# Kernel tuning notes

Hardware: AMD Instinct MI355X
Metric: run time of the kernel (lower is better)

The kernel has to match this reference:

```python
import jax, jax.numpy as jnp
import numpy as np

FP8_MAX = 448.0  # float8_e4m3fn max representable value


def _fp8_quant(v):
    """Snap values to the fp8 e4m3 grid (saturating), return fp32."""
    v = jnp.clip(v, -FP8_MAX, FP8_MAX)
    return v.astype(jnp.float8_e4m3fn).astype(jnp.float32)


def setup_inputs() -> dict:
    key = jax.random.key(0)
    k1, k2, k3 = jax.random.split(key, 3)
    N_TOK, D_IN, D_OUT = 8192, 4096, 4096
    x = jax.random.normal(k1, (N_TOK, D_IN), dtype=jnp.float32)
    # weight is stored already quantized to fp8 in the real module; snap to grid
    w = jax.random.normal(k2, (D_OUT, D_IN), dtype=jnp.float32)
    weight_scale = jnp.array([2.0 / FP8_MAX], dtype=jnp.float32)  # per-tensor
    weight = _fp8_quant(w / weight_scale)  # fp8-grid values, kept in fp32
    bias = jax.random.normal(k3, (D_OUT,), dtype=jnp.float32)
    input_scale = jnp.array([4.0 / FP8_MAX], dtype=jnp.float32)  # per-tensor act scale
    return {"x": x, "weight": weight, "weight_scale": weight_scale,
            "bias": bias, "input_scale": input_scale}


def reference(x, weight, weight_scale, bias, input_scale):
    # quantize_activation_per_tensor_fp8: x/scale -> clamp -> fp8 e4m3
    qinput = _fp8_quant(x / input_scale)  # [N, D_in], fp8-grid values
    acc = jnp.einsum('nk,ok->no', qinput, weight)  # fp32 accumulate
    out = acc * (input_scale * weight_scale) + bias
    return out.astype(x.dtype)
```

## Files before the change

kernel.cpp:

```cpp
#include <hip/hip_runtime.h>
#include <stdint.h>

#define FP8_MAX 448.0f

typedef float floatx4 __attribute__((ext_vector_type(4)));
typedef long  longx2  __attribute__((ext_vector_type(2)));

__device__ __forceinline__ void async_copy16(const void* g, void* s) {
    __builtin_amdgcn_global_load_lds(
        (const __attribute__((address_space(1))) void*)g,
        (__attribute__((address_space(3))) void*)s,
        16, 0, 0);
}

__global__ void __launch_bounds__(256) quant_fp8_kernel(
    const float* __restrict__ src, const float* __restrict__ scale,
    uint8_t* __restrict__ dst, long n16)
{
    long g = (long)blockIdx.x * 256 + threadIdx.x;
    if (g >= n16) return;
    long i = g * 16;
    float inv = 1.0f;
    if (scale) inv = 1.0f / scale[0];
    const float4* p = (const float4*)(src + i);
    int out[4];
#pragma unroll
    for (int j = 0; j < 4; ++j) {
        float4 v = p[j];
        float a = v.x * inv, b = v.y * inv, c = v.z * inv, d = v.w * inv;
        a = fminf(fmaxf(a, -FP8_MAX), FP8_MAX);
        b = fminf(fmaxf(b, -FP8_MAX), FP8_MAX);
        c = fminf(fmaxf(c, -FP8_MAX), FP8_MAX);
        d = fminf(fmaxf(d, -FP8_MAX), FP8_MAX);
        int pk = 0;
        pk = __builtin_amdgcn_cvt_pk_fp8_f32(a, b, pk, false);
        pk = __builtin_amdgcn_cvt_pk_fp8_f32(c, d, pk, true);
        out[j] = pk;
    }
    *(int4*)(dst + i) = make_int4(out[0], out[1], out[2], out[3]);
}

__global__ void __launch_bounds__(256, 2) gemm_fp8_kernel(
    const uint8_t* __restrict__ A, const uint8_t* __restrict__ B,
    const float* __restrict__ bias,
    const float* __restrict__ in_scale, const float* __restrict__ w_scale,
    float* __restrict__ C, int M, int N, int K)
{
    __shared__ __align__(16) uint8_t As[128 * 64];
    __shared__ __align__(16) uint8_t Bs[128 * 64];

    const int tid  = threadIdx.x;
    const int lane = tid & 63;
    const int wid  = tid >> 6;
    const int wm   = wid >> 1;
    const int wn   = wid & 1;
    const int m0   = blockIdx.y * 128;
    const int n0   = blockIdx.x * 128;

    const int mlane = lane & 15;
    const int quad  = lane >> 4;

    const int c0 = tid, c1 = tid + 256;
    const int rA0 = c0 >> 2, cA0 = (c0 & 3) * 16;
    const int rA1 = c1 >> 2, cA1 = (c1 & 3) * 16;

    const uint8_t* Ab = A + (size_t)m0 * K;
    const uint8_t* Bb = B + (size_t)n0 * K;

    floatx4 acc[4][4];
#pragma unroll
    for (int i = 0; i < 4; ++i)
#pragma unroll
        for (int j = 0; j < 4; ++j) acc[i][j] = (floatx4){0.f, 0.f, 0.f, 0.f};

    const int aoff = (wm * 64 + mlane) * 64 + quad * 16;
    const int boff = (wn * 64 + mlane) * 64 + quad * 16;

    for (int kt = 0; kt < K; kt += 64) {
        async_copy16(Ab + (size_t)rA0 * K + kt + cA0, As + c0 * 16);
        async_copy16(Ab + (size_t)rA1 * K + kt + cA1, As + c1 * 16);
        async_copy16(Bb + (size_t)rA0 * K + kt + cA0, Bs + c0 * 16);
        async_copy16(Bb + (size_t)rA1 * K + kt + cA1, Bs + c1 * 16);
        __syncthreads();

        longx2 av[4], bv[4];
#pragma unroll
        for (int mi = 0; mi < 4; ++mi)
            av[mi] = *(const longx2*)(As + aoff + mi * 16 * 64);
#pragma unroll
        for (int ni = 0; ni < 4; ++ni)
            bv[ni] = *(const longx2*)(Bs + boff + ni * 16 * 64);

#pragma unroll
        for (int mi = 0; mi < 4; ++mi)
#pragma unroll
            for (int ni = 0; ni < 4; ++ni)
                acc[mi][ni] = __builtin_amdgcn_mfma_f32_16x16x32_fp8_fp8(
                    av[mi].x, bv[ni].x, acc[mi][ni], 0, 0, 0);
#pragma unroll
        for (int mi = 0; mi < 4; ++mi)
#pragma unroll
            for (int ni = 0; ni < 4; ++ni)
                acc[mi][ni] = __builtin_amdgcn_mfma_f32_16x16x32_fp8_fp8(
                    av[mi].y, bv[ni].y, acc[mi][ni], 0, 0, 0);

        __syncthreads();
    }

    const float osc = in_scale[0] * w_scale[0];

#pragma unroll
    for (int mi = 0; mi < 4; ++mi) {
#pragma unroll
        for (int ni = 0; ni < 4; ++ni) {
            const int gn = n0 + wn * 64 + ni * 16 + mlane;
            const float bvv = bias[gn];
#pragma unroll
            for (int r = 0; r < 4; ++r) {
                const int gm = m0 + wm * 64 + mi * 16 + quad * 4 + r;
                C[(size_t)gm * N + gn] = acc[mi][ni][r] * osc + bvv;
            }
        }
    }
}

extern "C" void kernel_launch(void* const* d_in, const int* in_sizes, int n_in,
                              void* d_out, int out_size, void* d_ws, size_t ws_size,
                              hipStream_t stream) {
    const float* x        = (const float*)d_in[0];
    const float* weight   = (const float*)d_in[1];
    const float* w_scale  = (const float*)d_in[2];
    const float* bias     = (const float*)d_in[3];
    const float* in_scale = (const float*)d_in[4];
    float* out = (float*)d_out;

    const int N = in_sizes[3];
    const int K = in_sizes[1] / N;
    const int M = in_sizes[0] / K;

    uint8_t* qx = (uint8_t*)d_ws;
    uint8_t* qw = (uint8_t*)d_ws + (size_t)M * K;

    const long nx16 = (long)M * K / 16;
    const long nw16 = (long)N * K / 16;
    quant_fp8_kernel<<<(nx16 + 255) / 256, 256, 0, stream>>>(x, in_scale, qx, nx16);
    quant_fp8_kernel<<<(nw16 + 255) / 256, 256, 0, stream>>>(weight, nullptr, qw, nw16);

    dim3 grid(N / 128, M / 128);
    gemm_fp8_kernel<<<grid, 256, 0, stream>>>(qx, qw, bias, in_scale, w_scale,
                                              out, M, N, K);
}
```

Before: 434.3 us.

## Reorder LDS tile layout for conflict-free MFMA reads; grid-stride quant kernel

The GEMM's shared-memory tiles are reorganised so each 16-row by 64-byte MFMA sub-tile sits in a contiguous 1 KB block. Every lane then reads 16 consecutive bytes at lane*16 instead of striding by 64 bytes per row, which is meant to remove LDS bank conflicts on the fragment loads. The global-to-LDS copy mapping is changed to match, which makes each group of 16 threads fetch from 16 different rows. The quantization kernel becomes a grid-stride loop with one float4 per thread and a capped grid, trading wider 16-byte stores for narrower 4-byte stores.

```diff
diff --git a/kernel.cpp b/kernel.cpp
--- a/kernel.cpp
+++ b/kernel.cpp
@@ -15,29 +15,22 @@
 
 __global__ void __launch_bounds__(256) quant_fp8_kernel(
     const float* __restrict__ src, const float* __restrict__ scale,
-    uint8_t* __restrict__ dst, long n16)
+    uint8_t* __restrict__ dst, long n4)
 {
-    long g = (long)blockIdx.x * 256 + threadIdx.x;
-    if (g >= n16) return;
-    long i = g * 16;
     float inv = 1.0f;
     if (scale) inv = 1.0f / scale[0];
-    const float4* p = (const float4*)(src + i);
-    int out[4];
-#pragma unroll
-    for (int j = 0; j < 4; ++j) {
-        float4 v = p[j];
-        float a = v.x * inv, b = v.y * inv, c = v.z * inv, d = v.w * inv;
-        a = fminf(fmaxf(a, -FP8_MAX), FP8_MAX);
-        b = fminf(fmaxf(b, -FP8_MAX), FP8_MAX);
-        c = fminf(fmaxf(c, -FP8_MAX), FP8_MAX);
-        d = fminf(fmaxf(d, -FP8_MAX), FP8_MAX);
+    const long stride = (long)gridDim.x * 256;
+    for (long g = (long)blockIdx.x * 256 + threadIdx.x; g < n4; g += stride) {
+        float4 v = ((const float4*)src)[g];
+        float a = fminf(fmaxf(v.x * inv, -FP8_MAX), FP8_MAX);
+        float b = fminf(fmaxf(v.y * inv, -FP8_MAX), FP8_MAX);
+        float c = fminf(fmaxf(v.z * inv, -FP8_MAX), FP8_MAX);
+        float d = fminf(fmaxf(v.w * inv, -FP8_MAX), FP8_MAX);
         int pk = 0;
         pk = __builtin_amdgcn_cvt_pk_fp8_f32(a, b, pk, false);
         pk = __builtin_amdgcn_cvt_pk_fp8_f32(c, d, pk, true);
-        out[j] = pk;
+        ((int*)dst)[g] = pk;
     }
-    *(int4*)(dst + i) = make_int4(out[0], out[1], out[2], out[3]);
 }
 
 __global__ void __launch_bounds__(256, 2) gemm_fp8_kernel(
@@ -60,9 +53,9 @@
     const int mlane = lane & 15;
     const int quad  = lane >> 4;
 
-    const int c0 = tid, c1 = tid + 256;
-    const int rA0 = c0 >> 2, cA0 = (c0 & 3) * 16;
-    const int rA1 = c1 >> 2, cA1 = (c1 & 3) * 16;
+    const int S0 = tid, S1 = tid + 256;
+    const int rA0 = ((S0 >> 6) << 4) | (S0 & 15), cA0 = ((S0 >> 4) & 3) * 16;
+    const int rA1 = ((S1 >> 6) << 4) | (S1 & 15), cA1 = ((S1 >> 4) & 3) * 16;
 
     const uint8_t* Ab = A + (size_t)m0 * K;
     const uint8_t* Bb = B + (size_t)n0 * K;
@@ -73,23 +66,23 @@
 #pragma unroll
         for (int j = 0; j < 4; ++j) acc[i][j] = (floatx4){0.f, 0.f, 0.f, 0.f};
 
-    const int aoff = (wm * 64 + mlane) * 64 + quad * 16;
-    const int boff = (wn * 64 + mlane) * 64 + quad * 16;
+    const int aoff = (wm * 4) * 1024 + lane * 16;
+    const int boff = (wn * 4) * 1024 + lane * 16;
 
     for (int kt = 0; kt < K; kt += 64) {
-        async_copy16(Ab + (size_t)rA0 * K + kt + cA0, As + c0 * 16);
-        async_copy16(Ab + (size_t)rA1 * K + kt + cA1, As + c1 * 16);
-        async_copy16(Bb + (size_t)rA0 * K + kt + cA0, Bs + c0 * 16);
-        async_copy16(Bb + (size_t)rA1 * K + kt + cA1, Bs + c1 * 16);
+        async_copy16(Ab + (size_t)rA0 * K + kt + cA0, As + S0 * 16);
+        async_copy16(Ab + (size_t)rA1 * K + kt + cA1, As + S1 * 16);
+        async_copy16(Bb + (size_t)rA0 * K + kt + cA0, Bs + S0 * 16);
+        async_copy16(Bb + (size_t)rA1 * K + kt + cA1, Bs + S1 * 16);
         __syncthreads();
 
         longx2 av[4], bv[4];
 #pragma unroll
         for (int mi = 0; mi < 4; ++mi)
-            av[mi] = *(const longx2*)(As + aoff + mi * 16 * 64);
+            av[mi] = *(const longx2*)(As + aoff + mi * 1024);
 #pragma unroll
         for (int ni = 0; ni < 4; ++ni)
-            bv[ni] = *(const longx2*)(Bs + boff + ni * 16 * 64);
+            bv[ni] = *(const longx2*)(Bs + boff + ni * 1024);
 
 #pragma unroll
         for (int mi = 0; mi < 4; ++mi)
@@ -141,10 +134,12 @@
     uint8_t* qx = (uint8_t*)d_ws;
     uint8_t* qw = (uint8_t*)d_ws + (size_t)M * K;
 
-    const long nx16 = (long)M * K / 16;
-    const long nw16 = (long)N * K / 16;
-    quant_fp8_kernel<<<(nx16 + 255) / 256, 256, 0, stream>>>(x, in_scale, qx, nx16);
-    quant_fp8_kernel<<<(nw16 + 255) / 256, 256, 0, stream>>>(weight, nullptr, qw, nw16);
+    const long nx4 = (long)M * K / 4;
+    const long nw4 = (long)N * K / 4;
+    long bx = (nx4 + 255) / 256; if (bx > 2048) bx = 2048;
+    long bw = (nw4 + 255) / 256; if (bw > 2048) bw = 2048;
+    quant_fp8_kernel<<<(int)bx, 256, 0, stream>>>(x, in_scale, qx, nx4);
+    quant_fp8_kernel<<<(int)bw, 256, 0, stream>>>(weight, nullptr, qw, nw4);
 
     dim3 grid(N / 128, M / 128);
     gemm_fp8_kernel<<<grid, 256, 0, stream>>>(qx, qw, bias, in_scale, w_scale,
```

New measurement: 515.1 us. +18.6%, slower.
